# Kernel optimization log

Measured on AMD Instinct MI355X. Metric: run time of the kernel, lower is better.

The kernel has to match this reference:

```python
import jax, jax.numpy as jnp
import numpy as np

N, F_IN, H, C, E = 100000, 128, 128, 40, 600000


def setup_inputs() -> dict:
    key = jax.random.key(0)
    ks = jax.random.split(key, 20)
    s = 0.05
    inp = {
        "x": jax.random.normal(ks[0], (N, F_IN), jnp.float32),
        "edge_index": jax.random.randint(ks[1], (2, E), 0, N, jnp.int64),
        "importance": jnp.ones((F_IN,), jnp.float32),
        "W1": jax.random.normal(ks[2], (H, F_IN), jnp.float32) * s,
        "bl1": jax.random.normal(ks[3], (H,), jnp.float32) * s,
        "bc1": jnp.zeros((H,), jnp.float32),
        "W2": jax.random.normal(ks[4], (H, H), jnp.float32) * s,
        "bl2": jax.random.normal(ks[5], (H,), jnp.float32) * s,
        "bc2": jnp.zeros((H,), jnp.float32),
        "W3": jax.random.normal(ks[6], (H, H), jnp.float32) * s,
        "bl3": jax.random.normal(ks[7], (H,), jnp.float32) * s,
        "bc3": jnp.zeros((H,), jnp.float32),
        "Wlin1": jax.random.normal(ks[8], (H, H), jnp.float32) * s,
        "blin1": jax.random.normal(ks[9], (H,), jnp.float32) * s,
        "Wlin2": jax.random.normal(ks[10], (C, H), jnp.float32) * s,
        "blin2": jax.random.normal(ks[11], (C,), jnp.float32) * s,
    }
    return inp


def balanced_conv(x, W, bl, bc, row, col):
    # lin, then symmetric-normalized message, mean-aggregated over targets
    n = x.shape[0]
    h = x @ W.T + bl                                   # [N, H]
    loops = jnp.arange(n)
    r = jnp.concatenate([row, loops])                  # sources (x_j index)
    c = jnp.concatenate([col, loops])                  # targets
    deg = jnp.zeros((n,), x.dtype).at[c].add(1.0)      # degree(col) incl. self-loops
    dinv = deg ** -0.5
    norm = dinv[r] * dinv[c]                           # [E+N]
    msg = norm[:, None] * h[r]                         # gather + scale
    agg = jnp.zeros((n, h.shape[1]), x.dtype).at[c].add(msg)  # scatter-add
    return agg / deg[:, None] + bc                     # mean aggr + bias


def reference(x, edge_index, importance, W1, bl1, bc1, W2, bl2, bc2,
              W3, bl3, bc3, Wlin1, blin1, Wlin2, blin2):
    row, col = edge_index[0], edge_index[1]
    h = x * importance
    h = jax.nn.relu(balanced_conv(h, W1, bl1, bc1, row, col))
    h = jax.nn.relu(balanced_conv(h, W2, bl2, bc2, row, col))
    h = jax.nn.relu(balanced_conv(h, W3, bl3, bc3, row, col))
    h = jax.nn.relu(h @ Wlin1.T + blin1)
    h = h @ Wlin2.T + blin2
    return jax.nn.log_softmax(h, axis=-1)
```

## Files before the change

### kernel.cpp

```cpp
#include <hip/hip_runtime.h>
#include <hip/hip_bf16.h>

#define F 128
#define C_CLS 40
#define NWSPLIT 35
#define ELLCAP 32
#define NBKT 9

typedef __attribute__((ext_vector_type(8))) short short8;
typedef __attribute__((ext_vector_type(4))) float float4v;
typedef unsigned short ushort;

__device__ inline float bf2f(ushort u) {
  unsigned int x = ((unsigned int)u) << 16;
  return __builtin_bit_cast(float, x);
}
__device__ inline ushort f2bf(float f) {
  __hip_bfloat16 h = __float2bfloat16(f);
  return __builtin_bit_cast(ushort, h);
}
__device__ inline void split_bf16(float f, ushort& hi, ushort& lo) {
  hi = f2bf(f);
  lo = f2bf(f - bf2f(hi));
}
__device__ inline int swz(int lane) { return lane ^ ((lane >> 4) & 3); }
__device__ inline int bucket_of(int cv) {
  int lim = cv < ELLCAP ? cv : ELLCAP;
  int nIt = (lim + 3) >> 2;
  return 8 - nIt;
}

__global__ __launch_bounds__(256) void setup_kernel(
    const float* __restrict__ W1, const float* __restrict__ imp,
    const float* __restrict__ W2, const float* __restrict__ W3,
    const float* __restrict__ Wl1, const float* __restrict__ Wh2,
    ushort* __restrict__ WhP,
    ushort* __restrict__ W2hH, ushort* __restrict__ W2lH,
    const int* __restrict__ row, const int* __restrict__ col,
    int* __restrict__ cnt, int* __restrict__ ell,
    int ne, int n) {
  int b = blockIdx.x;
  if (b < NWSPLIT) {
    int ci = b * 256 + threadIdx.x;
    if (ci < 8192) {
      const float* src[4] = {W1, W2, W3, Wl1};
      int p = ci >> 11, c = ci & 2047;
      int kc = c >> 10, ct = (c >> 7) & 7, ks = (c >> 6) & 1, ln = c & 63;
      int dl = swz(ln);
      int colw = ct * 16 + (dl & 15);
      int k = kc * 64 + ks * 32 + (dl >> 4) * 8;
      float4 f0 = *(const float4*)&src[p][(size_t)colw * F + k];
      float4 f1 = *(const float4*)&src[p][(size_t)colw * F + k + 4];
      float v[8] = {f0.x, f0.y, f0.z, f0.w, f1.x, f1.y, f1.z, f1.w};
      if (p == 0) {
        float4 i0 = *(const float4*)&imp[k];
        float4 i1 = *(const float4*)&imp[k + 4];
        v[0] *= i0.x; v[1] *= i0.y; v[2] *= i0.z; v[3] *= i0.w;
        v[4] *= i1.x; v[5] *= i1.y; v[6] *= i1.z; v[7] *= i1.w;
      }
      ushort hi[8];
#pragma unroll
      for (int j = 0; j < 8; ++j) hi[j] = f2bf(v[j]);
      *(short8*)&WhP[(size_t)ci * 8] = *(short8*)hi;
    } else if (ci < 8192 + 768) {
      int c = ci - 8192;
      int ct = c >> 8, ks = (c >> 6) & 3, ln = c & 63;
      int colw = ct * 16 + (ln & 15);
      int k = ks * 32 + (ln >> 4) * 8;
      float v[8];
      if (colw < C_CLS) {
        float4 f0 = *(const float4*)&Wh2[(size_t)colw * F + k];
        float4 f1 = *(const float4*)&Wh2[(size_t)colw * F + k + 4];
        v[0] = f0.x; v[1] = f0.y; v[2] = f0.z; v[3] = f0.w;
        v[4] = f1.x; v[5] = f1.y; v[6] = f1.z; v[7] = f1.w;
      } else {
#pragma unroll
        for (int j = 0; j < 8; ++j) v[j] = 0.f;
      }
      ushort hi[8], lo[8];
#pragma unroll
      for (int j = 0; j < 8; ++j) split_bf16(v[j], hi[j], lo[j]);
      *(short8*)&W2hH[(size_t)c * 8] = *(short8*)hi;
      *(short8*)&W2lH[(size_t)c * 8] = *(short8*)lo;
    }
  } else {
    int e = (b - NWSPLIT) * 256 + threadIdx.x;
    if (e < ne) {
      int r = row[e], c = col[e];
      int p = atomicAdd(&cnt[c], 1);
      if (p < ELLCAP) ell[(size_t)c * ELLCAP + p] = r;
    }
  }
}

__global__ __launch_bounds__(256) void prepass_kernel(
    const float* __restrict__ x, const int* __restrict__ cnt,
    int* __restrict__ ell, float* __restrict__ wsum, int* __restrict__ hist,
    ushort* __restrict__ Xs, ushort* __restrict__ Az,
    int n, int nbW, int nbX) {
  int b = blockIdx.x;
  if (b < nbW) {
    __shared__ int lh[NBKT];
    int t = threadIdx.x;
    if (t < NBKT) lh[t] = 0;
    __syncthreads();
    int node = b * 256 + t;
    if (node < n) {
      int cv = cnt[node];
      int lim = cv < ELLCAP ? cv : ELLCAP;
      int lim4 = (lim + 3) & ~3;
      float gs = 0.f;
      const int4* ep = (const int4*)&ell[(size_t)node * ELLCAP];
      for (int base = 0; base < lim; base += 4) {
        int4 rr = ep[base >> 2];
        bool p1 = base + 1 < lim, p2 = base + 2 < lim, p3 = base + 3 < lim;
        int r1 = p1 ? rr.y : rr.x;
        int r2 = p2 ? rr.z : rr.x;
        int r3 = p3 ? rr.w : rr.x;
        float g0 = rsqrtf((float)(cnt[rr.x] + 1));
        float g1 = p1 ? rsqrtf((float)(cnt[r1] + 1)) : 0.f;
        float g2 = p2 ? rsqrtf((float)(cnt[r2] + 1)) : 0.f;
        float g3 = p3 ? rsqrtf((float)(cnt[r3] + 1)) : 0.f;
        gs += (g0 + g1) + (g2 + g3);
      }
      float d = (float)(cv + 1);
      wsum[node] = rsqrtf(d) * gs + 1.0f / d;
      for (int p = lim; p < lim4; ++p) ell[(size_t)node * ELLCAP + p] = n;
      atomicAdd(&lh[bucket_of(cv)], 1);
    }
    __syncthreads();
    if (t < NBKT) atomicAdd(&hist[t], lh[t]);
  } else if (b < nbW + nbX) {
    size_t i = (size_t)(b - nbW) * 2048 + (size_t)threadIdx.x * 8;
    if (i < (size_t)n * F) {
      int node = (int)(i >> 7);
      float dc = rsqrtf((float)(cnt[node] + 1));
      float4 f0 = *(const float4*)&x[i];
      float4 f1 = *(const float4*)&x[i + 4];
      ushort o[8] = {f2bf(dc * f0.x), f2bf(dc * f0.y), f2bf(dc * f0.z), f2bf(dc * f0.w),
                     f2bf(dc * f1.x), f2bf(dc * f1.y), f2bf(dc * f1.z), f2bf(dc * f1.w)};
      *(short8*)&Xs[i] = *(short8*)o;
    }
  } else {
    int t = threadIdx.x;
    short8 z = (short8){0, 0, 0, 0, 0, 0, 0, 0};
    if (t < 16) *(short8*)&Xs[(size_t)n * F + t * 8] = z;
    else if (t < 32) *(short8*)&Az[(size_t)n * F + (t - 16) * 8] = z;
  }
}

__global__ __launch_bounds__(256) void perm_kernel(
    const int* __restrict__ cnt, const int* __restrict__ hist,
    int* __restrict__ cursor, int* __restrict__ perm, int n) {
  __shared__ int lh[NBKT], lbase[NBKT];
  int t = threadIdx.x;
  if (t < NBKT) lh[t] = 0;
  __syncthreads();
  int node = blockIdx.x * 256 + t;
  int bkt = 0, idx = 0;
  if (node < n) {
    bkt = bucket_of(cnt[node]);
    idx = atomicAdd(&lh[bkt], 1);
  }
  __syncthreads();
  if (t < NBKT) {
    int pre = 0;
#pragma unroll
    for (int k = 0; k < NBKT; ++k)
      if (k < t) pre += hist[k];
    lbase[t] = pre + atomicAdd(&cursor[t], lh[t]);
  }
  __syncthreads();
  if (node < n) perm[lbase[bkt] + idx] = node;
}

__global__ __launch_bounds__(256) void conv_fused(
    const int* __restrict__ cnt, const int* __restrict__ ell,
    const int* __restrict__ perm,
    const ushort* __restrict__ Xs, const ushort* __restrict__ Wh,
    const float* __restrict__ wsum, const float* __restrict__ bl,
    const float* __restrict__ bc, ushort* __restrict__ OUT, int n) {
  const int t = threadIdx.x;
  const int w = t >> 6, lane = t & 63, quad = lane >> 4, cl = lane & 15;
  const int gid = blockIdx.x * 64 + w * 16 + cl;
  const bool valid = gid < n;
  const int node = valid ? perm[gid] : 0;

  float acc[4][8];
#pragma unroll
  for (int ks = 0; ks < 4; ++ks)
#pragma unroll
    for (int q = 0; q < 8; ++q) acc[ks][q] = 0.f;

  float dc = 1.f, id = 1.f;
  int nIt = 0;
  if (valid) {
    int cv = cnt[node];
    float d = (float)(cv + 1);
    dc = rsqrtf(d);
    id = 1.0f / d;
    int lim = cv < ELLCAP ? cv : ELLCAP;
    nIt = (lim + 3) >> 2;
  }
  const int4* ep = (const int4*)&ell[(size_t)node * ELLCAP];
  const int qoff = quad * 8;

  if (nIt > 0) {
    int4 rr = ep[0];
    for (int it = 0; it < nIt; ++it) {
      const ushort* r0 = &Xs[(size_t)rr.x * F + qoff];
      const ushort* r1 = &Xs[(size_t)rr.y * F + qoff];
      const ushort* r2 = &Xs[(size_t)rr.z * F + qoff];
      const ushort* r3 = &Xs[(size_t)rr.w * F + qoff];
      short8 v[4][4];
#pragma unroll
      for (int ks = 0; ks < 4; ++ks) {
        v[0][ks] = *(const short8*)&r0[ks * 32];
        v[1][ks] = *(const short8*)&r1[ks * 32];
        v[2][ks] = *(const short8*)&r2[ks * 32];
        v[3][ks] = *(const short8*)&r3[ks * 32];
      }
      int jn = (it + 1 < nIt) ? it + 1 : it;
      rr = ep[jn];
#pragma unroll
      for (int ks = 0; ks < 4; ++ks)
#pragma unroll
        for (int q = 0; q < 8; ++q) {
          float t0 = bf2f((ushort)v[0][ks][q]) + bf2f((ushort)v[1][ks][q]);
          float t1 = bf2f((ushort)v[2][ks][q]) + bf2f((ushort)v[3][ks][q]);
          acc[ks][q] += t0 + t1;
        }
    }
  }

  short8 sfrag[4];
  if (valid) {
    const ushort* sq = &Xs[(size_t)node * F + qoff];
#pragma unroll
    for (int ks = 0; ks < 4; ++ks) {
      short8 sv = *(const short8*)&sq[ks * 32];
      ushort o[8];
#pragma unroll
      for (int q = 0; q < 8; ++q)
        o[q] = f2bf(dc * (acc[ks][q] + bf2f((ushort)sv[q])));
      sfrag[ks] = *(short8*)o;
    }
  } else {
#pragma unroll
    for (int ks = 0; ks < 4; ++ks) sfrag[ks] = (short8){0, 0, 0, 0, 0, 0, 0, 0};
  }

  float4v co[8];
#pragma unroll
  for (int mt = 0; mt < 8; ++mt) co[mt] = (float4v){0.f, 0.f, 0.f, 0.f};
  const int sl = swz(lane);
#pragma unroll
  for (int ks = 0; ks < 4; ++ks) {
    const int base2 = ((ks >> 1) * 1024 + (ks & 1) * 64 + sl) * 8;
#pragma unroll
    for (int mt = 0; mt < 8; ++mt) {
      short8 a_h = *(const short8*)&Wh[base2 + mt * 1024];
      co[mt] = __builtin_amdgcn_mfma_f32_16x16x32_bf16(a_h, sfrag[ks], co[mt], 0, 0, 0);
    }
  }

  if (valid) {
    float ws = wsum[node];
#pragma unroll
    for (int mt = 0; mt < 8; ++mt) {
      float4 blv = *(const float4*)&bl[mt * 16 + quad * 4];
      float4 bcv = *(const float4*)&bc[mt * 16 + quad * 4];
      float v0 = fmaxf((co[mt][0] + ws * blv.x) * id + bcv.x, 0.f) * dc;
      float v1 = fmaxf((co[mt][1] + ws * blv.y) * id + bcv.y, 0.f) * dc;
      float v2 = fmaxf((co[mt][2] + ws * blv.z) * id + bcv.z, 0.f) * dc;
      float v3 = fmaxf((co[mt][3] + ws * blv.w) * id + bcv.w, 0.f) * dc;
      ushort o[4] = {f2bf(v0), f2bf(v1), f2bf(v2), f2bf(v3)};
      *(ushort4*)&OUT[(size_t)node * F + mt * 16 + quad * 4] = *(ushort4*)o;
    }
  }
}

__global__ __launch_bounds__(256) void conv_head(
    const int* __restrict__ cnt, const int* __restrict__ ell,
    const int* __restrict__ perm,
    const ushort* __restrict__ Xs, const ushort* __restrict__ Wh3,
    const float* __restrict__ wsum, const float* __restrict__ bl3,
    const float* __restrict__ bc3,
    const ushort* __restrict__ Wl1h, const float* __restrict__ bli1,
    const ushort* __restrict__ W2h, const ushort* __restrict__ W2l,
    const float* __restrict__ b2, float* __restrict__ out, int n) {
  __shared__ ushort sH[8192];
  const int t = threadIdx.x;
  const int w = t >> 6, lane = t & 63, quad = lane >> 4, cl = lane & 15;
  const int sl = swz(lane);
  const int qoff = quad * 8;
  char* sHb = (char*)sH;

  const int gid = blockIdx.x * 64 + w * 16 + cl;
  const bool valid = gid < n;
  const int node = valid ? perm[gid] : 0;

  float acc[4][8];
#pragma unroll
  for (int ks = 0; ks < 4; ++ks)
#pragma unroll
    for (int q = 0; q < 8; ++q) acc[ks][q] = 0.f;

  float dc = 1.f, id = 1.f, ws = 0.f;
  int nIt = 0;
  if (valid) {
    int cv = cnt[node];
    float d = (float)(cv + 1);
    dc = rsqrtf(d);
    id = 1.0f / d;
    ws = wsum[node];
    int lim = cv < ELLCAP ? cv : ELLCAP;
    nIt = (lim + 3) >> 2;
  }
  const int4* ep = (const int4*)&ell[(size_t)node * ELLCAP];

  if (nIt > 0) {
    int4 rr = ep[0];
    for (int it = 0; it < nIt; ++it) {
      const ushort* r0 = &Xs[(size_t)rr.x * F + qoff];
      const ushort* r1 = &Xs[(size_t)rr.y * F + qoff];
      const ushort* r2 = &Xs[(size_t)rr.z * F + qoff];
      const ushort* r3 = &Xs[(size_t)rr.w * F + qoff];
      short8 v[4][4];
#pragma unroll
      for (int ks = 0; ks < 4; ++ks) {
        v[0][ks] = *(const short8*)&r0[ks * 32];
        v[1][ks] = *(const short8*)&r1[ks * 32];
        v[2][ks] = *(const short8*)&r2[ks * 32];
        v[3][ks] = *(const short8*)&r3[ks * 32];
      }
      int jn = (it + 1 < nIt) ? it + 1 : it;
      rr = ep[jn];
#pragma unroll
      for (int ks = 0; ks < 4; ++ks)
#pragma unroll
        for (int q = 0; q < 8; ++q) {
          float t0 = bf2f((ushort)v[0][ks][q]) + bf2f((ushort)v[1][ks][q]);
          float t1 = bf2f((ushort)v[2][ks][q]) + bf2f((ushort)v[3][ks][q]);
          acc[ks][q] += t0 + t1;
        }
    }
  }

  short8 sfrag[4];
  if (valid) {
    const ushort* sq = &Xs[(size_t)node * F + qoff];
#pragma unroll
    for (int ks = 0; ks < 4; ++ks) {
      short8 sv = *(const short8*)&sq[ks * 32];
      ushort o[8];
#pragma unroll
      for (int q = 0; q < 8; ++q)
        o[q] = f2bf(dc * (acc[ks][q] + bf2f((ushort)sv[q])));
      sfrag[ks] = *(short8*)o;
    }
  } else {
#pragma unroll
    for (int ks = 0; ks < 4; ++ks) sfrag[ks] = (short8){0, 0, 0, 0, 0, 0, 0, 0};
  }

  float4v co[8];
#pragma unroll
  for (int mt = 0; mt < 8; ++mt) co[mt] = (float4v){0.f, 0.f, 0.f, 0.f};
#pragma unroll
  for (int ks = 0; ks < 4; ++ks) {
    const int base2 = ((ks >> 1) * 1024 + (ks & 1) * 64 + sl) * 8;
#pragma unroll
    for (int mt = 0; mt < 8; ++mt) {
      short8 a_h = *(const short8*)&Wh3[base2 + mt * 1024];
      co[mt] = __builtin_amdgcn_mfma_f32_16x16x32_bf16(a_h, sfrag[ks], co[mt], 0, 0, 0);
    }
  }

#pragma unroll
  for (int mt = 0; mt < 8; ++mt) {
    float4 blv = *(const float4*)&bl3[mt * 16 + quad * 4];
    float4 bcv = *(const float4*)&bc3[mt * 16 + quad * 4];
    ushort o[4];
    o[0] = f2bf(fmaxf((co[mt][0] + ws * blv.x) * id + bcv.x, 0.f));
    o[1] = f2bf(fmaxf((co[mt][1] + ws * blv.y) * id + bcv.y, 0.f));
    o[2] = f2bf(fmaxf((co[mt][2] + ws * blv.z) * id + bcv.z, 0.f));
    o[3] = f2bf(fmaxf((co[mt][3] + ws * blv.w) * id + bcv.w, 0.f));
    int ch = (mt * 2 + (quad >> 1)) ^ cl;
    *(ushort4*)&sHb[w * 4096 + cl * 256 + ch * 16 + (quad & 1) * 8] = *(ushort4*)o;
  }

  float4v acc1[8];
#pragma unroll
  for (int mt = 0; mt < 8; ++mt) acc1[mt] = (float4v){0.f, 0.f, 0.f, 0.f};
#pragma unroll
  for (int ks = 0; ks < 4; ++ks) {
    int ch2 = (ks * 4 + quad) ^ cl;
    short8 bfr = *(short8*)&sHb[w * 4096 + cl * 256 + ch2 * 16];
    const int base2 = ((ks >> 1) * 1024 + (ks & 1) * 64 + sl) * 8;
#pragma unroll
    for (int mt = 0; mt < 8; ++mt) {
      short8 a_h = *(const short8*)&Wl1h[base2 + mt * 1024];
      acc1[mt] = __builtin_amdgcn_mfma_f32_16x16x32_bf16(a_h, bfr, acc1[mt], 0, 0, 0);
    }
  }

#pragma unroll
  for (int mt = 0; mt < 8; ++mt) {
    float4 bv = *(const float4*)&bli1[mt * 16 + quad * 4];
    ushort o[4];
    o[0] = f2bf(fmaxf(acc1[mt][0] + bv.x, 0.f));
    o[1] = f2bf(fmaxf(acc1[mt][1] + bv.y, 0.f));
    o[2] = f2bf(fmaxf(acc1[mt][2] + bv.z, 0.f));
    o[3] = f2bf(fmaxf(acc1[mt][3] + bv.w, 0.f));
    int ch = (mt * 2 + (quad >> 1)) ^ cl;
    *(ushort4*)&sHb[w * 4096 + cl * 256 + ch * 16 + (quad & 1) * 8] = *(ushort4*)o;
  }

  float4v accl[3];
#pragma unroll
  for (int ct = 0; ct < 3; ++ct) accl[ct] = (float4v){0.f, 0.f, 0.f, 0.f};
#pragma unroll
  for (int ks = 0; ks < 4; ++ks) {
    int ch2 = (ks * 4 + quad) ^ cl;
    short8 a = *(short8*)&sHb[w * 4096 + cl * 256 + ch2 * 16];
#pragma unroll
    for (int ct = 0; ct < 3; ++ct) {
      int chunk = ((ct * 4 + ks) * 64 + lane) * 8;
      short8 b_h = *(const short8*)&W2h[chunk];
      short8 b_l = *(const short8*)&W2l[chunk];
      accl[ct] = __builtin_amdgcn_mfma_f32_16x16x32_bf16(a, b_h, accl[ct], 0, 0, 0);
      accl[ct] = __builtin_amdgcn_mfma_f32_16x16x32_bf16(a, b_l, accl[ct], 0, 0, 0);
    }
  }

  float b0 = b2[cl];
  float b1 = b2[16 + cl];
  float b2v = (32 + cl < C_CLS) ? b2[32 + cl] : -1e30f;
  float lse[4];
#pragma unroll
  for (int reg = 0; reg < 4; ++reg) {
    float v0 = accl[0][reg] + b0;
    float v1 = accl[1][reg] + b1;
    float v2 = accl[2][reg] + b2v;
    accl[0][reg] = v0; accl[1][reg] = v1; accl[2][reg] = v2;
    float m = fmaxf(fmaxf(v0, v1), v2);
#pragma unroll
    for (int o = 1; o < 16; o <<= 1) m = fmaxf(m, __shfl_xor(m, o));
    float s = __expf(v0 - m) + __expf(v1 - m) + __expf(v2 - m);
#pragma unroll
    for (int o = 1; o < 16; o <<= 1) s += __shfl_xor(s, o);
    lse[reg] = logf(s) + m;
  }
  int vn = valid ? node : -1;
#pragma unroll
  for (int reg = 0; reg < 4; ++reg) {
    int s = quad * 4 + reg;
    int gn = __shfl(vn, s);
    if (gn >= 0) {
      out[(size_t)gn * C_CLS + cl] = accl[0][reg] - lse[reg];
      out[(size_t)gn * C_CLS + 16 + cl] = accl[1][reg] - lse[reg];
      if (cl < 8) out[(size_t)gn * C_CLS + 32 + cl] = accl[2][reg] - lse[reg];
    }
  }
}

extern "C" void kernel_launch(void* const* d_in, const int* in_sizes, int n_in,
                              void* d_out, int out_size, void* d_ws, size_t ws_size,
                              hipStream_t stream) {
  const float* x    = (const float*)d_in[0];
  const int*   ei   = (const int*)d_in[1];
  const float* imp  = (const float*)d_in[2];
  const float* W1   = (const float*)d_in[3];
  const float* bl1  = (const float*)d_in[4];
  const float* bc1  = (const float*)d_in[5];
  const float* W2   = (const float*)d_in[6];
  const float* bl2  = (const float*)d_in[7];
  const float* bc2  = (const float*)d_in[8];
  const float* W3   = (const float*)d_in[9];
  const float* bl3  = (const float*)d_in[10];
  const float* bc3  = (const float*)d_in[11];
  const float* Wl1  = (const float*)d_in[12];
  const float* bli1 = (const float*)d_in[13];
  const float* Wl2  = (const float*)d_in[14];
  const float* bli2 = (const float*)d_in[15];
  float* out = (float*)d_out;

  const int N = in_sizes[0] / F;
  const int E = in_sizes[1] / 2;

  ushort* A16 = (ushort*)d_ws;
  ushort* B16 = A16 + (size_t)(N + 1) * F;
  ushort* WhP = B16 + (size_t)(N + 1) * F;
  ushort* W2hH = WhP + 65536;
  ushort* W2lH = W2hH + 6144;
  float* wsum = (float*)(W2lH + 6144);
  int*   cnt  = (int*)(wsum + N);
  int*   hist = cnt + N;
  int*   cursor = hist + NBKT;
  int*   perm = cursor + NBKT;
  int*   ell  = perm + N;

  const int* rowv = ei;
  const int* colv = ei + E;

  int nbE  = (E + 255) / 256;
  int nbW  = (N + 255) / 256;
  int nbX  = (N * F + 2047) / 2048;
  int nbCv = (N + 63) / 64;

  hipMemsetAsync(cnt, 0, ((size_t)N + 2 * NBKT) * sizeof(int), stream);
  setup_kernel<<<NWSPLIT + nbE, 256, 0, stream>>>(
      W1, imp, W2, W3, Wl1, Wl2, WhP, W2hH, W2lH, rowv, colv, cnt, ell, E, N);
  prepass_kernel<<<nbW + nbX + 1, 256, 0, stream>>>(
      x, cnt, ell, wsum, hist, B16, A16, N, nbW, nbX);
  perm_kernel<<<nbW, 256, 0, stream>>>(cnt, hist, cursor, perm, N);

  conv_fused<<<nbCv, 256, 0, stream>>>(cnt, ell, perm, B16, WhP,         wsum, bl1, bc1, A16, N);
  conv_fused<<<nbCv, 256, 0, stream>>>(cnt, ell, perm, A16, WhP + 16384, wsum, bl2, bc2, B16, N);

  conv_head<<<nbCv, 256, 0, stream>>>(cnt, ell, perm, B16, WhP + 32768, wsum, bl3, bc3,
                                      WhP + 49152, bli1, W2hH, W2lH, bli2, out, N);
}
```

Before: 351.2 us.

## Split fused gather+GEMM conv into lean gather kernel and separate GEMM kernels

Each fused conv layer (neighbor gather-sum followed by MFMA GEMM) becomes two kernels. A lean gather kernel uses 16 threads per node with 16-byte loads and four independent accumulators, writing the normalized aggregate to a scratch buffer. A GEMM kernel then reads rows in natural order and applies the bias, ReLU and normalization. This cuts register pressure in the gather so more loads can be in flight, and it makes the head's output writes contiguous. In exchange it adds an extra round trip of the full N x 128 bf16 intermediate through memory per layer, plus extra kernel launches.

```diff
diff --git a/kernel.cpp b/kernel.cpp
--- a/kernel.cpp
+++ b/kernel.cpp
@@ -174,80 +174,65 @@
   if (node < n) perm[lbase[bkt] + idx] = node;
 }
 
-__global__ __launch_bounds__(256) void conv_fused(
+__global__ __launch_bounds__(256) void gather_lean(
     const int* __restrict__ cnt, const int* __restrict__ ell,
     const int* __restrict__ perm,
-    const ushort* __restrict__ Xs, const ushort* __restrict__ Wh,
-    const float* __restrict__ wsum, const float* __restrict__ bl,
-    const float* __restrict__ bc, ushort* __restrict__ OUT, int n) {
+    const ushort* __restrict__ Xin, ushort* __restrict__ S, int n) {
+  int g = blockIdx.x * 16 + (threadIdx.x >> 4);
+  if (g >= n) return;
+  int node = perm[g];
+  int j = (threadIdx.x & 15) * 8;
+  int cv = cnt[node];
+  float dc = rsqrtf((float)(cv + 1));
+  int lim = cv < ELLCAP ? cv : ELLCAP;
+  int lim4 = (lim + 3) & ~3;
+  const int4* ep = (const int4*)&ell[(size_t)node * ELLCAP];
+  float a0[8] = {0, 0, 0, 0, 0, 0, 0, 0};
+  float a1[8] = {0, 0, 0, 0, 0, 0, 0, 0};
+  float a2[8] = {0, 0, 0, 0, 0, 0, 0, 0};
+  float a3[8] = {0, 0, 0, 0, 0, 0, 0, 0};
+  for (int base = 0; base < lim4; base += 4) {
+    int4 rr = ep[base >> 2];
+    short8 v0 = *(const short8*)&Xin[(size_t)rr.x * F + j];
+    short8 v1 = *(const short8*)&Xin[(size_t)rr.y * F + j];
+    short8 v2 = *(const short8*)&Xin[(size_t)rr.z * F + j];
+    short8 v3 = *(const short8*)&Xin[(size_t)rr.w * F + j];
+#pragma unroll
+    for (int q = 0; q < 8; ++q) {
+      a0[q] += bf2f((ushort)v0[q]);
+      a1[q] += bf2f((ushort)v1[q]);
+      a2[q] += bf2f((ushort)v2[q]);
+      a3[q] += bf2f((ushort)v3[q]);
+    }
+  }
+  short8 sv = *(const short8*)&Xin[(size_t)node * F + j];
+  ushort o[8];
+#pragma unroll
+  for (int q = 0; q < 8; ++q) {
+    float s = (a0[q] + a1[q]) + (a2[q] + a3[q]) + bf2f((ushort)sv[q]);
+    o[q] = f2bf(dc * s);
+  }
+  *(short8*)&S[(size_t)node * F + j] = *(short8*)o;
+}
+
+__global__ __launch_bounds__(256) void gemm_mid(
+    const ushort* __restrict__ S, const ushort* __restrict__ Wh,
+    const int* __restrict__ cnt, const float* __restrict__ wsum,
+    const float* __restrict__ bl, const float* __restrict__ bc,
+    ushort* __restrict__ OUT, int n) {
   const int t = threadIdx.x;
   const int w = t >> 6, lane = t & 63, quad = lane >> 4, cl = lane & 15;
-  const int gid = blockIdx.x * 64 + w * 16 + cl;
-  const bool valid = gid < n;
-  const int node = valid ? perm[gid] : 0;
-
-  float acc[4][8];
-#pragma unroll
-  for (int ks = 0; ks < 4; ++ks)
-#pragma unroll
-    for (int q = 0; q < 8; ++q) acc[ks][q] = 0.f;
-
-  float dc = 1.f, id = 1.f;
-  int nIt = 0;
+  const int gr = blockIdx.x * 64 + w * 16 + cl;
+  const bool valid = gr < n;
+
+  short8 b[4];
   if (valid) {
-    int cv = cnt[node];
-    float d = (float)(cv + 1);
-    dc = rsqrtf(d);
-    id = 1.0f / d;
-    int lim = cv < ELLCAP ? cv : ELLCAP;
-    nIt = (lim + 3) >> 2;
-  }
-  const int4* ep = (const int4*)&ell[(size_t)node * ELLCAP];
-  const int qoff = quad * 8;
-
-  if (nIt > 0) {
-    int4 rr = ep[0];
-    for (int it = 0; it < nIt; ++it) {
-      const ushort* r0 = &Xs[(size_t)rr.x * F + qoff];
-      const ushort* r1 = &Xs[(size_t)rr.y * F + qoff];
-      const ushort* r2 = &Xs[(size_t)rr.z * F + qoff];
-      const ushort* r3 = &Xs[(size_t)rr.w * F + qoff];
-      short8 v[4][4];
-#pragma unroll
-      for (int ks = 0; ks < 4; ++ks) {
-        v[0][ks] = *(const short8*)&r0[ks * 32];
-        v[1][ks] = *(const short8*)&r1[ks * 32];
-        v[2][ks] = *(const short8*)&r2[ks * 32];
-        v[3][ks] = *(const short8*)&r3[ks * 32];
-      }
-      int jn = (it + 1 < nIt) ? it + 1 : it;
-      rr = ep[jn];
-#pragma unroll
-      for (int ks = 0; ks < 4; ++ks)
-#pragma unroll
-        for (int q = 0; q < 8; ++q) {
-          float t0 = bf2f((ushort)v[0][ks][q]) + bf2f((ushort)v[1][ks][q]);
-          float t1 = bf2f((ushort)v[2][ks][q]) + bf2f((ushort)v[3][ks][q]);
-          acc[ks][q] += t0 + t1;
-        }
-    }
-  }
-
-  short8 sfrag[4];
-  if (valid) {
-    const ushort* sq = &Xs[(size_t)node * F + qoff];
-#pragma unroll
-    for (int ks = 0; ks < 4; ++ks) {
-      short8 sv = *(const short8*)&sq[ks * 32];
-      ushort o[8];
-#pragma unroll
-      for (int q = 0; q < 8; ++q)
-        o[q] = f2bf(dc * (acc[ks][q] + bf2f((ushort)sv[q])));
-      sfrag[ks] = *(short8*)o;
-    }
+    const ushort* sq = &S[(size_t)gr * F + quad * 8];
+#pragma unroll
+    for (int ks = 0; ks < 4; ++ks) b[ks] = *(const short8*)&sq[ks * 32];
   } else {
 #pragma unroll
-    for (int ks = 0; ks < 4; ++ks) sfrag[ks] = (short8){0, 0, 0, 0, 0, 0, 0, 0};
+    for (int ks = 0; ks < 4; ++ks) b[ks] = (short8){0, 0, 0, 0, 0, 0, 0, 0};
   }
 
   float4v co[8];
@@ -260,12 +245,15 @@
 #pragma unroll
     for (int mt = 0; mt < 8; ++mt) {
       short8 a_h = *(const short8*)&Wh[base2 + mt * 1024];
-      co[mt] = __builtin_amdgcn_mfma_f32_16x16x32_bf16(a_h, sfrag[ks], co[mt], 0, 0, 0);
+      co[mt] = __builtin_amdgcn_mfma_f32_16x16x32_bf16(a_h, b[ks], co[mt], 0, 0, 0);
     }
   }
 
   if (valid) {
-    float ws = wsum[node];
+    float d = (float)(cnt[gr] + 1);
+    float dc = rsqrtf(d);
+    float id = 1.0f / d;
+    float ws = wsum[gr];
 #pragma unroll
     for (int mt = 0; mt < 8; ++mt) {
       float4 blv = *(const float4*)&bl[mt * 16 + quad * 4];
@@ -275,17 +263,15 @@
       float v2 = fmaxf((co[mt][2] + ws * blv.z) * id + bcv.z, 0.f) * dc;
       float v3 = fmaxf((co[mt][3] + ws * blv.w) * id + bcv.w, 0.f) * dc;
       ushort o[4] = {f2bf(v0), f2bf(v1), f2bf(v2), f2bf(v3)};
-      *(ushort4*)&OUT[(size_t)node * F + mt * 16 + quad * 4] = *(ushort4*)o;
-    }
-  }
-}
-
-__global__ __launch_bounds__(256) void conv_head(
-    const int* __restrict__ cnt, const int* __restrict__ ell,
-    const int* __restrict__ perm,
-    const ushort* __restrict__ Xs, const ushort* __restrict__ Wh3,
-    const float* __restrict__ wsum, const float* __restrict__ bl3,
-    const float* __restrict__ bc3,
+      *(ushort4*)&OUT[(size_t)gr * F + mt * 16 + quad * 4] = *(ushort4*)o;
+    }
+  }
+}
+
+__global__ __launch_bounds__(256) void head3(
+    const ushort* __restrict__ S, const ushort* __restrict__ Wh3,
+    const int* __restrict__ cnt, const float* __restrict__ wsum,
+    const float* __restrict__ bl3, const float* __restrict__ bc3,
     const ushort* __restrict__ Wl1h, const float* __restrict__ bli1,
     const ushort* __restrict__ W2h, const ushort* __restrict__ W2l,
     const float* __restrict__ b2, float* __restrict__ out, int n) {
@@ -293,75 +279,23 @@
   const int t = threadIdx.x;
   const int w = t >> 6, lane = t & 63, quad = lane >> 4, cl = lane & 15;
   const int sl = swz(lane);
-  const int qoff = quad * 8;
   char* sHb = (char*)sH;
 
-  const int gid = blockIdx.x * 64 + w * 16 + cl;
-  const bool valid = gid < n;
-  const int node = valid ? perm[gid] : 0;
-
-  float acc[4][8];
-#pragma unroll
-  for (int ks = 0; ks < 4; ++ks)
-#pragma unroll
-    for (int q = 0; q < 8; ++q) acc[ks][q] = 0.f;
-
-  float dc = 1.f, id = 1.f, ws = 0.f;
-  int nIt = 0;
+  const int row0 = blockIdx.x * 64 + w * 16;
+  const int gr = row0 + cl;
+  const bool valid = gr < n;
+
+  short8 b[4];
+  float id = 1.f, ws = 0.f;
   if (valid) {
-    int cv = cnt[node];
-    float d = (float)(cv + 1);
-    dc = rsqrtf(d);
-    id = 1.0f / d;
-    ws = wsum[node];
-    int lim = cv < ELLCAP ? cv : ELLCAP;
-    nIt = (lim + 3) >> 2;
-  }
-  const int4* ep = (const int4*)&ell[(size_t)node * ELLCAP];
-
-  if (nIt > 0) {
-    int4 rr = ep[0];
-    for (int it = 0; it < nIt; ++it) {
-      const ushort* r0 = &Xs[(size_t)rr.x * F + qoff];
-      const ushort* r1 = &Xs[(size_t)rr.y * F + qoff];
-      const ushort* r2 = &Xs[(size_t)rr.z * F + qoff];
-      const ushort* r3 = &Xs[(size_t)rr.w * F + qoff];
-      short8 v[4][4];
-#pragma unroll
-      for (int ks = 0; ks < 4; ++ks) {
-        v[0][ks] = *(const short8*)&r0[ks * 32];
-        v[1][ks] = *(const short8*)&r1[ks * 32];
-        v[2][ks] = *(const short8*)&r2[ks * 32];
-        v[3][ks] = *(const short8*)&r3[ks * 32];
-      }
-      int jn = (it + 1 < nIt) ? it + 1 : it;
-      rr = ep[jn];
-#pragma unroll
-      for (int ks = 0; ks < 4; ++ks)
-#pragma unroll
-        for (int q = 0; q < 8; ++q) {
-          float t0 = bf2f((ushort)v[0][ks][q]) + bf2f((ushort)v[1][ks][q]);
-          float t1 = bf2f((ushort)v[2][ks][q]) + bf2f((ushort)v[3][ks][q]);
-          acc[ks][q] += t0 + t1;
-        }
-    }
-  }
-
-  short8 sfrag[4];
-  if (valid) {
-    const ushort* sq = &Xs[(size_t)node * F + qoff];
-#pragma unroll
-    for (int ks = 0; ks < 4; ++ks) {
-      short8 sv = *(const short8*)&sq[ks * 32];
-      ushort o[8];
-#pragma unroll
-      for (int q = 0; q < 8; ++q)
-        o[q] = f2bf(dc * (acc[ks][q] + bf2f((ushort)sv[q])));
-      sfrag[ks] = *(short8*)o;
-    }
+    const ushort* sq = &S[(size_t)gr * F + quad * 8];
+#pragma unroll
+    for (int ks = 0; ks < 4; ++ks) b[ks] = *(const short8*)&sq[ks * 32];
+    id = 1.0f / (float)(cnt[gr] + 1);
+    ws = wsum[gr];
   } else {
 #pragma unroll
-    for (int ks = 0; ks < 4; ++ks) sfrag[ks] = (short8){0, 0, 0, 0, 0, 0, 0, 0};
+    for (int ks = 0; ks < 4; ++ks) b[ks] = (short8){0, 0, 0, 0, 0, 0, 0, 0};
   }
 
   float4v co[8];
@@ -373,7 +307,7 @@
 #pragma unroll
     for (int mt = 0; mt < 8; ++mt) {
       short8 a_h = *(const short8*)&Wh3[base2 + mt * 1024];
-      co[mt] = __builtin_amdgcn_mfma_f32_16x16x32_bf16(a_h, sfrag[ks], co[mt], 0, 0, 0);
+      co[mt] = __builtin_amdgcn_mfma_f32_16x16x32_bf16(a_h, b[ks], co[mt], 0, 0, 0);
     }
   }
 
@@ -452,15 +386,13 @@
     for (int o = 1; o < 16; o <<= 1) s += __shfl_xor(s, o);
     lse[reg] = logf(s) + m;
   }
-  int vn = valid ? node : -1;
 #pragma unroll
   for (int reg = 0; reg < 4; ++reg) {
-    int s = quad * 4 + reg;
-    int gn = __shfl(vn, s);
-    if (gn >= 0) {
-      out[(size_t)gn * C_CLS + cl] = accl[0][reg] - lse[reg];
-      out[(size_t)gn * C_CLS + 16 + cl] = accl[1][reg] - lse[reg];
-      if (cl < 8) out[(size_t)gn * C_CLS + 32 + cl] = accl[2][reg] - lse[reg];
+    int go = row0 + quad * 4 + reg;
+    if (go < n) {
+      out[(size_t)go * C_CLS + cl] = accl[0][reg] - lse[reg];
+      out[(size_t)go * C_CLS + 16 + cl] = accl[1][reg] - lse[reg];
+      if (cl < 8) out[(size_t)go * C_CLS + 32 + cl] = accl[2][reg] - lse[reg];
     }
   }
 }
@@ -507,7 +439,8 @@
   int nbE  = (E + 255) / 256;
   int nbW  = (N + 255) / 256;
   int nbX  = (N * F + 2047) / 2048;
-  int nbCv = (N + 63) / 64;
+  int nbGa = (N + 15) / 16;
+  int nbGe = (N + 63) / 64;
 
   hipMemsetAsync(cnt, 0, ((size_t)N + 2 * NBKT) * sizeof(int), stream);
   setup_kernel<<<NWSPLIT + nbE, 256, 0, stream>>>(
@@ -516,9 +449,13 @@
       x, cnt, ell, wsum, hist, B16, A16, N, nbW, nbX);
   perm_kernel<<<nbW, 256, 0, stream>>>(cnt, hist, cursor, perm, N);
 
-  conv_fused<<<nbCv, 256, 0, stream>>>(cnt, ell, perm, B16, WhP,         wsum, bl1, bc1, A16, N);
-  conv_fused<<<nbCv, 256, 0, stream>>>(cnt, ell, perm, A16, WhP + 16384, wsum, bl2, bc2, B16, N);
-
-  conv_head<<<nbCv, 256, 0, stream>>>(cnt, ell, perm, B16, WhP + 32768, wsum, bl3, bc3,
-                                      WhP + 49152, bli1, W2hH, W2lH, bli2, out, N);
-}
+  gather_lean<<<nbGa, 256, 0, stream>>>(cnt, ell, perm, B16, A16, N);
+  gemm_mid<<<nbGe, 256, 0, stream>>>(A16, WhP, cnt, wsum, bl1, bc1, B16, N);
+
+  gather_lean<<<nbGa, 256, 0, stream>>>(cnt, ell, perm, B16, A16, N);
+  gemm_mid<<<nbGe, 256, 0, stream>>>(A16, WhP + 16384, cnt, wsum, bl2, bc2, B16, N);
+
+  gather_lean<<<nbGa, 256, 0, stream>>>(cnt, ell, perm, B16, A16, N);
+  head3<<<nbGe, 256, 0, stream>>>(A16, WhP + 32768, cnt, wsum, bl3, bc3,
+                                  WhP + 49152, bli1, W2hH, W2lH, bli2, out, N);
+}
```

Result: faster. 338.9 us (-3.5%).
